# Performance work log

Measured on AMD Instinct MI355X. Metric: run time of the kernel, lower is better.

The kernel has to match this reference:

```python
import jax, jax.numpy as jnp
import numpy as np

NG, NT, E = 2500, 20000, 640000
SRC_DIM, DST_DIM, HID, OUT, NCLS = 128, 500, 128, 128, 16


def setup_inputs() -> dict:
    key = jax.random.key(0)
    ks = jax.random.split(key, 11)
    d = {
        "gene_feats": jax.random.normal(ks[0], (NG, SRC_DIM), jnp.float32),
        "train_feats": jax.random.normal(ks[1], (NT, DST_DIM), jnp.float32),
        "edge_src": jax.random.randint(ks[2], (E,), 0, NG),
        "edge_dst": jax.random.randint(ks[3], (E,), 0, NT),
        # conv1: SAGEConv((src_dim, dst_dim) -> hidden)
        "W1_neigh": jax.random.normal(ks[4], (SRC_DIM, HID), jnp.float32) / np.sqrt(SRC_DIM),
        "W1_self": jax.random.normal(ks[5], (DST_DIM, HID), jnp.float32) / np.sqrt(DST_DIM),
        "b1": jnp.zeros((HID,), jnp.float32),
        # conv2: SAGEConv(hidden -> out); src input is the raw gene features
        "W2_neigh": jax.random.normal(ks[6], (HID, OUT), jnp.float32) / np.sqrt(HID),
        "W2_self": jax.random.normal(ks[7], (HID, OUT), jnp.float32) / np.sqrt(HID),
        "b2": jnp.zeros((OUT,), jnp.float32),
        # classifier MLP
        "Wc1": jax.random.normal(ks[8], (OUT, OUT), jnp.float32) / np.sqrt(OUT),
        "bc1": jnp.zeros((OUT,), jnp.float32),
        "Wc2": jax.random.normal(ks[9], (OUT, NCLS), jnp.float32) / np.sqrt(OUT),
        "bc2": jnp.zeros((NCLS,), jnp.float32),
    }
    return d


def _segment_mean(msgs, dst, num_segments):
    # mean over in-edges; isolated dst nodes get 0 (DGL convention)
    sums = jax.ops.segment_sum(msgs, dst, num_segments=num_segments)
    cnt = jax.ops.segment_sum(jnp.ones((msgs.shape[0],), msgs.dtype), dst,
                              num_segments=num_segments)
    return sums / jnp.maximum(cnt, 1.0)[:, None]


def reference(gene_feats, train_feats, edge_src, edge_dst,
              W1_neigh, W1_self, b1, W2_neigh, W2_self, b2,
              Wc1, bc1, Wc2, bc2):
    # mean-aggregate gene (src) features onto train (dst) nodes
    agg = _segment_mean(gene_feats[edge_src], edge_dst, NT)  # [NT, SRC_DIM]
    # conv1: fc_self(h_dst) + fc_neigh(mean_neigh) + bias, then ReLU
    h1 = jax.nn.relu(train_feats @ W1_self + agg @ W1_neigh + b1)  # [NT, HID]
    # conv2 reuses raw gene features as src -> same mean aggregation
    h2 = jax.nn.relu(h1 @ W2_self + agg @ W2_neigh + b2)  # [NT, OUT]
    # classifier: Linear -> ReLU -> Linear
    return jax.nn.relu(h2 @ Wc1 + bc1) @ Wc2 + bc2  # [NT, NCLS]
```

## Files before the change

### kernel.cpp

```cpp
#include <hip/hip_runtime.h>


#define NG 2500
#define NT 20000
#define NE 640000
#define NCLS 16
#define CAP 96

typedef unsigned short u16;
typedef unsigned int u32;

typedef float f32x4 __attribute__((ext_vector_type(4)));
typedef __bf16 bf16x8 __attribute__((ext_vector_type(8)));

__device__ __forceinline__ float b2f(u16 u) { return __uint_as_float(((u32)u) << 16); }
__device__ __forceinline__ float blo(u32 p) { return __uint_as_float(p << 16); }
__device__ __forceinline__ float bhi(u32 p) { return __uint_as_float(p & 0xffff0000u); }
__device__ __forceinline__ u16 f2b(float f) {
    u32 u = __float_as_uint(f);
    return (u16)((u + 0x7fffu + ((u >> 16) & 1u)) >> 16);
}

#define B1N 81920
#define B2N 32768
#define B3N 16384
#define B4N 2048
#define NEB 625
#define GNB 625
#define PKB 520

__global__ __launch_bounds__(256) void k_prep(
    const int* __restrict__ esrc, const int* __restrict__ edst,
    int* __restrict__ cnt, u16* __restrict__ csr,
    const float* __restrict__ gene, u32* __restrict__ GH32,
    const float* __restrict__ W1n, const float* __restrict__ W1s,
    const float* __restrict__ W2n, const float* __restrict__ W2s,
    const float* __restrict__ Wc1, const float* __restrict__ Wc2,
    u16* __restrict__ B1h, u16* __restrict__ B1l,
    u16* __restrict__ B2h, u16* __restrict__ B2l,
    u16* __restrict__ B3h, u16* __restrict__ B3l,
    u16* __restrict__ B4h, u16* __restrict__ B4l) {
    int blk = blockIdx.x, t = threadIdx.x;
    if (blk < NEB) {
        int e0 = (blk * 256 + t) * 4;
        const int4 s4 = *(const int4*)(esrc + e0);
        const int4 d4 = *(const int4*)(edst + e0);
        int ss[4] = {s4.x, s4.y, s4.z, s4.w};
        int dd[4] = {d4.x, d4.y, d4.z, d4.w};
#pragma unroll
        for (int i = 0; i < 4; ++i) {
            unsigned d = (unsigned)dd[i];
            if (d < NT) {
                int slot = atomicAdd(&cnt[d], 1);
                if (slot < CAP) csr[(size_t)d * CAP + slot] = (u16)ss[i];
            }
        }
        return;
    }
    if (blk < NEB + GNB) {
        int idx = (blk - NEB) * 256 + t;
        float2 v = ((const float2*)gene)[idx];
        GH32[idx] = (u32)f2b(v.x) | ((u32)f2b(v.y) << 16);
        return;
    }
    int idx = (blk - NEB - GNB) * 256 + t;
    float v = 0.f;
    u16 *ph = 0, *pl = 0;
    int off = 0;
    if (idx < B1N) {
        int j = idx & 7, l = (idx >> 3) & 63, rest = idx >> 9;
        int g = rest & 7, kk = rest >> 3;
        int k = kk * 32 + ((l >> 4) << 3) + j, n = (g << 4) + (l & 15);
        if (k < 500) v = W1s[k * 128 + n];
        else if (k >= 512) v = W1n[(k - 512) * 128 + n];
        ph = B1h; pl = B1l; off = idx;
    } else if (idx < B1N + B2N) {
        int e = idx - B1N;
        int j = e & 7, l = (e >> 3) & 63, rest = e >> 9;
        int g = rest & 7, kk = rest >> 3;
        int k = kk * 32 + ((l >> 4) << 3) + j, n = (g << 4) + (l & 15);
        v = (k < 128) ? W2s[k * 128 + n] : W2n[(k - 128) * 128 + n];
        ph = B2h; pl = B2l; off = e;
    } else if (idx < B1N + B2N + B3N) {
        int e = idx - (B1N + B2N);
        int j = e & 7, l = (e >> 3) & 63, rest = e >> 9;
        int g = rest & 7, kk = rest >> 3;
        int k = kk * 32 + ((l >> 4) << 3) + j, n = (g << 4) + (l & 15);
        v = Wc1[k * 128 + n];
        ph = B3h; pl = B3l; off = e;
    } else if (idx < B1N + B2N + B3N + B4N) {
        int e = idx - (B1N + B2N + B3N);
        int j = e & 7, l = (e >> 3) & 63, kk = e >> 9;
        int k = kk * 32 + ((l >> 4) << 3) + j, n = l & 15;
        v = Wc2[k * 16 + n];
        ph = B4h; pl = B4l; off = e;
    }
    if (ph) {
        u16 hi = f2b(v);
        u16 lo = f2b(v - b2f(hi));
        ph[off] = hi;
        pl[off] = lo;
    }
}

__global__ __launch_bounds__(512) void k_mega(
    const int* __restrict__ cnt, const u16* __restrict__ csr,
    const u16* __restrict__ GH, const float* __restrict__ train,
    const u16* __restrict__ B1h, const u16* __restrict__ B1l,
    const u16* __restrict__ B2h, const u16* __restrict__ B2l,
    const u16* __restrict__ B3h, const u16* __restrict__ B3l,
    const u16* __restrict__ B4h, const u16* __restrict__ B4l,
    const float* __restrict__ b1, const float* __restrict__ b2,
    const float* __restrict__ bc1, const float* __restrict__ bc2,
    float* __restrict__ out) {
    __shared__ __align__(16) u16 SMEM[26112];
    u16* SAGh = SMEM;
    u16* SAGl = SMEM + 4352;
    u16* S1h = SMEM + 8704;
    u16* S1l = SMEM + 13056;
    u16* S2h = SMEM + 17408;
    u16* S2l = SMEM + 21760;
    u16* TS = SMEM + 8704;

    int t = threadIdx.x;
    int row0 = blockIdx.x * 32;

    float4 st[8];
    {
        const float4* tb = (const float4*)(train + (size_t)row0 * 500);
#pragma unroll
        for (int i = 0; i < 7; ++i) st[i] = tb[t + i * 512];
        if (t < 416) st[7] = tb[t + 3584];
    }

    {
        int r = t >> 4, cg = t & 15;
        int d = row0 + r;
        int ctrue = cnt[d];
        int c = ctrue > CAP ? CAP : ctrue;
        const u16* crow = csr + (size_t)d * CAP;
        float a[8];
#pragma unroll
        for (int p = 0; p < 8; ++p) a[p] = 0.f;
        int j = 0;
        for (; j + 1 < c; j += 2) {
            int s0 = crow[j], s1 = crow[j + 1];
            uint4 p0 = *(const uint4*)(GH + (size_t)s0 * 128 + cg * 8);
            uint4 p1 = *(const uint4*)(GH + (size_t)s1 * 128 + cg * 8);
            a[0] += blo(p0.x); a[1] += bhi(p0.x);
            a[2] += blo(p0.y); a[3] += bhi(p0.y);
            a[4] += blo(p0.z); a[5] += bhi(p0.z);
            a[6] += blo(p0.w); a[7] += bhi(p0.w);
            a[0] += blo(p1.x); a[1] += bhi(p1.x);
            a[2] += blo(p1.y); a[3] += bhi(p1.y);
            a[4] += blo(p1.z); a[5] += bhi(p1.z);
            a[6] += blo(p1.w); a[7] += bhi(p1.w);
        }
        if (j < c) {
            int s = crow[j];
            uint4 p0 = *(const uint4*)(GH + (size_t)s * 128 + cg * 8);
            a[0] += blo(p0.x); a[1] += bhi(p0.x);
            a[2] += blo(p0.y); a[3] += bhi(p0.y);
            a[4] += blo(p0.z); a[5] += bhi(p0.z);
            a[6] += blo(p0.w); a[7] += bhi(p0.w);
        }
        float inv = (ctrue > 0) ? 1.f / (float)ctrue : 0.f;
        int base = (r * 136 + cg * 8) >> 1;
        u32* SH = (u32*)SAGh;
        u32* SL = (u32*)SAGl;
#pragma unroll
        for (int p = 0; p < 4; ++p) {
            float x = a[2 * p] * inv, y = a[2 * p + 1] * inv;
            u16 hx = f2b(x), hy = f2b(y);
            SH[base + p] = (u32)hx | ((u32)hy << 16);
            SL[base + p] = (u32)f2b(x - b2f(hx)) | ((u32)f2b(y - b2f(hy)) << 16);
        }
    }

    {
        u32* T32 = (u32*)TS;
#pragma unroll
        for (int i = 0; i < 8; ++i) {
            int idx = t + i * 512;
            if (i == 7 && t >= 416) break;
            int r = idx / 125, c4 = idx - r * 125;
            int base = r * 260 + c4 * 2;
            T32[base] = (u32)f2b(st[i].x) | ((u32)f2b(st[i].y) << 16);
            T32[base + 1] = (u32)f2b(st[i].z) | ((u32)f2b(st[i].w) << 16);
        }
        if (t < 192) {
            int r = t / 6, c = t - r * 6;
            T32[r * 260 + 250 + c] = 0;
        }
    }
    __syncthreads();

    int lane = t & 63, g = t >> 6;
    int m = lane & 15, q = lane >> 4, n16 = lane & 15;

    int hr0 = m * 136 + q * 8;
    int hr1 = (16 + m) * 136 + q * 8;
    int cr0 = q * 4, cr1 = 16 + q * 4;
    const f32x4 z4 = {0.f, 0.f, 0.f, 0.f};
    f32x4 acc0 = z4, acc1 = z4;

    const u16* tA0 = TS + m * 520 + q * 8;
    const u16* tA1 = TS + (16 + m) * 520 + q * 8;
#pragma unroll
    for (int kk = 0; kk < 16; ++kk) {
        bf16x8 a0 = *(const bf16x8*)(tA0 + kk * 32);
        bf16x8 a1 = *(const bf16x8*)(tA1 + kk * 32);
        size_t bo = ((size_t)(kk * 8 + g) * 64 + lane) * 8;
        bf16x8 bh = *(const bf16x8*)(B1h + bo);
        bf16x8 bl = *(const bf16x8*)(B1l + bo);
        acc0 = __builtin_amdgcn_mfma_f32_16x16x32_bf16(a0, bh, acc0, 0, 0, 0);
        acc0 = __builtin_amdgcn_mfma_f32_16x16x32_bf16(a0, bl, acc0, 0, 0, 0);
        acc1 = __builtin_amdgcn_mfma_f32_16x16x32_bf16(a1, bh, acc1, 0, 0, 0);
        acc1 = __builtin_amdgcn_mfma_f32_16x16x32_bf16(a1, bl, acc1, 0, 0, 0);
    }
#pragma unroll
    for (int kk = 16; kk < 20; ++kk) {
        int o = (kk - 16) * 32;
        bf16x8 ah0 = *(const bf16x8*)(SAGh + hr0 + o);
        bf16x8 al0 = *(const bf16x8*)(SAGl + hr0 + o);
        bf16x8 ah1 = *(const bf16x8*)(SAGh + hr1 + o);
        bf16x8 al1 = *(const bf16x8*)(SAGl + hr1 + o);
        size_t bo = ((size_t)(kk * 8 + g) * 64 + lane) * 8;
        bf16x8 bh = *(const bf16x8*)(B1h + bo);
        bf16x8 bl = *(const bf16x8*)(B1l + bo);
        acc0 = __builtin_amdgcn_mfma_f32_16x16x32_bf16(ah0, bh, acc0, 0, 0, 0);
        acc0 = __builtin_amdgcn_mfma_f32_16x16x32_bf16(ah0, bl, acc0, 0, 0, 0);
        acc0 = __builtin_amdgcn_mfma_f32_16x16x32_bf16(al0, bh, acc0, 0, 0, 0);
        acc1 = __builtin_amdgcn_mfma_f32_16x16x32_bf16(ah1, bh, acc1, 0, 0, 0);
        acc1 = __builtin_amdgcn_mfma_f32_16x16x32_bf16(ah1, bl, acc1, 0, 0, 0);
        acc1 = __builtin_amdgcn_mfma_f32_16x16x32_bf16(al1, bh, acc1, 0, 0, 0);
    }
    __syncthreads();
    {
        int n = g * 16 + n16;
        float bias = b1[n];
#pragma unroll
        for (int rg = 0; rg < 4; ++rg) {
            float v0 = acc0[rg] + bias; v0 = v0 > 0.f ? v0 : 0.f;
            float v1 = acc1[rg] + bias; v1 = v1 > 0.f ? v1 : 0.f;
            u16 h0 = f2b(v0), h1v = f2b(v1);
            S1h[(cr0 + rg) * 136 + n] = h0; S1l[(cr0 + rg) * 136 + n] = f2b(v0 - b2f(h0));
            S1h[(cr1 + rg) * 136 + n] = h1v; S1l[(cr1 + rg) * 136 + n] = f2b(v1 - b2f(h1v));
        }
    }
    __syncthreads();

    acc0 = z4; acc1 = z4;
#pragma unroll
    for (int kk = 0; kk < 8; ++kk) {
        const u16* Ph = (kk < 4) ? S1h : SAGh;
        const u16* Pl = (kk < 4) ? S1l : SAGl;
        int o = (kk & 3) * 32;
        bf16x8 ah0 = *(const bf16x8*)(Ph + hr0 + o);
        bf16x8 al0 = *(const bf16x8*)(Pl + hr0 + o);
        bf16x8 ah1 = *(const bf16x8*)(Ph + hr1 + o);
        bf16x8 al1 = *(const bf16x8*)(Pl + hr1 + o);
        size_t bo = ((size_t)(kk * 8 + g) * 64 + lane) * 8;
        bf16x8 bh = *(const bf16x8*)(B2h + bo);
        bf16x8 bl = *(const bf16x8*)(B2l + bo);
        acc0 = __builtin_amdgcn_mfma_f32_16x16x32_bf16(ah0, bh, acc0, 0, 0, 0);
        acc0 = __builtin_amdgcn_mfma_f32_16x16x32_bf16(ah0, bl, acc0, 0, 0, 0);
        acc0 = __builtin_amdgcn_mfma_f32_16x16x32_bf16(al0, bh, acc0, 0, 0, 0);
        acc1 = __builtin_amdgcn_mfma_f32_16x16x32_bf16(ah1, bh, acc1, 0, 0, 0);
        acc1 = __builtin_amdgcn_mfma_f32_16x16x32_bf16(ah1, bl, acc1, 0, 0, 0);
        acc1 = __builtin_amdgcn_mfma_f32_16x16x32_bf16(al1, bh, acc1, 0, 0, 0);
    }
    {
        int n = g * 16 + n16;
        float bias = b2[n];
#pragma unroll
        for (int rg = 0; rg < 4; ++rg) {
            float v0 = acc0[rg] + bias; v0 = v0 > 0.f ? v0 : 0.f;
            float v1 = acc1[rg] + bias; v1 = v1 > 0.f ? v1 : 0.f;
            u16 h0 = f2b(v0), h1v = f2b(v1);
            S2h[(cr0 + rg) * 136 + n] = h0; S2l[(cr0 + rg) * 136 + n] = f2b(v0 - b2f(h0));
            S2h[(cr1 + rg) * 136 + n] = h1v; S2l[(cr1 + rg) * 136 + n] = f2b(v1 - b2f(h1v));
        }
    }
    __syncthreads();

    acc0 = z4; acc1 = z4;
#pragma unroll
    for (int kk = 0; kk < 4; ++kk) {
        int o = kk * 32;
        bf16x8 ah0 = *(const bf16x8*)(S2h + hr0 + o);
        bf16x8 al0 = *(const bf16x8*)(S2l + hr0 + o);
        bf16x8 ah1 = *(const bf16x8*)(S2h + hr1 + o);
        bf16x8 al1 = *(const bf16x8*)(S2l + hr1 + o);
        size_t bo = ((size_t)(kk * 8 + g) * 64 + lane) * 8;
        bf16x8 bh = *(const bf16x8*)(B3h + bo);
        bf16x8 bl = *(const bf16x8*)(B3l + bo);
        acc0 = __builtin_amdgcn_mfma_f32_16x16x32_bf16(ah0, bh, acc0, 0, 0, 0);
        acc0 = __builtin_amdgcn_mfma_f32_16x16x32_bf16(ah0, bl, acc0, 0, 0, 0);
        acc0 = __builtin_amdgcn_mfma_f32_16x16x32_bf16(al0, bh, acc0, 0, 0, 0);
        acc1 = __builtin_amdgcn_mfma_f32_16x16x32_bf16(ah1, bh, acc1, 0, 0, 0);
        acc1 = __builtin_amdgcn_mfma_f32_16x16x32_bf16(ah1, bl, acc1, 0, 0, 0);
        acc1 = __builtin_amdgcn_mfma_f32_16x16x32_bf16(al1, bh, acc1, 0, 0, 0);
    }
    {
        int n = g * 16 + n16;
        float bias = bc1[n];
#pragma unroll
        for (int rg = 0; rg < 4; ++rg) {
            float v0 = acc0[rg] + bias; v0 = v0 > 0.f ? v0 : 0.f;
            float v1 = acc1[rg] + bias; v1 = v1 > 0.f ? v1 : 0.f;
            u16 h0 = f2b(v0), h1v = f2b(v1);
            S1h[(cr0 + rg) * 136 + n] = h0; S1l[(cr0 + rg) * 136 + n] = f2b(v0 - b2f(h0));
            S1h[(cr1 + rg) * 136 + n] = h1v; S1l[(cr1 + rg) * 136 + n] = f2b(v1 - b2f(h1v));
        }
    }
    __syncthreads();

    if (g < 2) {
        int hr = (g == 0) ? hr0 : hr1;
        int cr = (g == 0) ? cr0 : cr1;
        f32x4 a4 = z4;
#pragma unroll
        for (int kk = 0; kk < 4; ++kk) {
            bf16x8 ah = *(const bf16x8*)(S1h + hr + kk * 32);
            bf16x8 al = *(const bf16x8*)(S1l + hr + kk * 32);
            size_t bo = ((size_t)kk * 64 + lane) * 8;
            bf16x8 bh = *(const bf16x8*)(B4h + bo);
            bf16x8 bl = *(const bf16x8*)(B4l + bo);
            a4 = __builtin_amdgcn_mfma_f32_16x16x32_bf16(ah, bh, a4, 0, 0, 0);
            a4 = __builtin_amdgcn_mfma_f32_16x16x32_bf16(ah, bl, a4, 0, 0, 0);
            a4 = __builtin_amdgcn_mfma_f32_16x16x32_bf16(al, bh, a4, 0, 0, 0);
        }
        float bias = bc2[n16];
#pragma unroll
        for (int rg = 0; rg < 4; ++rg)
            out[(size_t)(row0 + cr + rg) * NCLS + n16] = a4[rg] + bias;
    }
}

extern "C" void kernel_launch(void* const* d_in, const int* in_sizes, int n_in,
                              void* d_out, int out_size, void* d_ws, size_t ws_size,
                              hipStream_t stream) {
    const float* gene = (const float*)d_in[0];
    const float* train = (const float*)d_in[1];
    const int* esrc = (const int*)d_in[2];
    const int* edst = (const int*)d_in[3];

    char* ws = (char*)d_ws;
    int* cnt = (int*)(ws + 0);
    u16* csr = (u16*)(ws + 80000);
    u16* GH = (u16*)(ws + 3920000);
    u16* B1h = (u16*)(ws + 4560000);
    u16* B1l = (u16*)(ws + 4723840);
    u16* B2h = (u16*)(ws + 4887680);
    u16* B2l = (u16*)(ws + 4953216);
    u16* B3h = (u16*)(ws + 5018752);
    u16* B3l = (u16*)(ws + 5051520);
    u16* B4h = (u16*)(ws + 5084288);
    u16* B4l = (u16*)(ws + 5088384);

    hipMemsetAsync(cnt, 0, NT * sizeof(int), stream);
    k_prep<<<NEB + GNB + PKB, 256, 0, stream>>>(
        esrc, edst, cnt, csr, gene, (u32*)GH,
        (const float*)d_in[4], (const float*)d_in[5], (const float*)d_in[7],
        (const float*)d_in[8], (const float*)d_in[10], (const float*)d_in[12],
        B1h, B1l, B2h, B2l, B3h, B3l, B4h, B4l);
    k_mega<<<NT / 32, 512, 0, stream>>>(
        cnt, csr, GH, train, B1h, B1l, B2h, B2l, B3h, B3l, B4h, B4l,
        (const float*)d_in[6], (const float*)d_in[9], (const float*)d_in[11],
        (const float*)d_in[13], (float*)d_out);
}
```

Before: 167.6 us.

## Halve rows per block in fused GNN kernel and batch eight edges per thread

The fused kernel now processes 16 destination rows per 512-thread block instead of 32. That halves shared memory and register use and doubles the grid to 1250 blocks for better occupancy and load balance. The trade-off is that each block reloads the full weight tiles for half as many rows, which doubles weight traffic per row, and each MFMA stage now has a single accumulator chain. Separately, the edge-bucketing phase handles eight edges per thread with fewer blocks.

```diff
diff --git a/kernel.cpp b/kernel.cpp
--- a/kernel.cpp
+++ b/kernel.cpp
@@ -25,7 +25,7 @@
 #define B2N 32768
 #define B3N 16384
 #define B4N 2048
-#define NEB 625
+#define NEB 313
 #define GNB 625
 #define PKB 520
 
@@ -42,17 +42,21 @@
     u16* __restrict__ B4h, u16* __restrict__ B4l) {
     int blk = blockIdx.x, t = threadIdx.x;
     if (blk < NEB) {
-        int e0 = (blk * 256 + t) * 4;
-        const int4 s4 = *(const int4*)(esrc + e0);
-        const int4 d4 = *(const int4*)(edst + e0);
-        int ss[4] = {s4.x, s4.y, s4.z, s4.w};
-        int dd[4] = {d4.x, d4.y, d4.z, d4.w};
-#pragma unroll
-        for (int i = 0; i < 4; ++i) {
-            unsigned d = (unsigned)dd[i];
-            if (d < NT) {
-                int slot = atomicAdd(&cnt[d], 1);
-                if (slot < CAP) csr[(size_t)d * CAP + slot] = (u16)ss[i];
+        int e0 = (blk * 256 + t) * 8;
+        if (e0 < NE) {
+            int4 sA = *(const int4*)(esrc + e0);
+            int4 sB = *(const int4*)(esrc + e0 + 4);
+            int4 dA = *(const int4*)(edst + e0);
+            int4 dB = *(const int4*)(edst + e0 + 4);
+            int ss[8] = {sA.x, sA.y, sA.z, sA.w, sB.x, sB.y, sB.z, sB.w};
+            int dd[8] = {dA.x, dA.y, dA.z, dA.w, dB.x, dB.y, dB.z, dB.w};
+#pragma unroll
+            for (int i = 0; i < 8; ++i) {
+                unsigned d = (unsigned)dd[i];
+                if (d < NT) {
+                    int slot = atomicAdd(&cnt[d], 1);
+                    if (slot < CAP) csr[(size_t)d * CAP + slot] = (u16)ss[i];
+                }
             }
         }
         return;
@@ -113,82 +117,96 @@
     const float* __restrict__ b1, const float* __restrict__ b2,
     const float* __restrict__ bc1, const float* __restrict__ bc2,
     float* __restrict__ out) {
-    __shared__ __align__(16) u16 SMEM[26112];
+    __shared__ __align__(16) u16 SMEM[13056];
     u16* SAGh = SMEM;
-    u16* SAGl = SMEM + 4352;
-    u16* S1h = SMEM + 8704;
-    u16* S1l = SMEM + 13056;
-    u16* S2h = SMEM + 17408;
-    u16* S2l = SMEM + 21760;
-    u16* TS = SMEM + 8704;
+    u16* SAGl = SMEM + 2176;
+    u16* S1h = SMEM + 4352;
+    u16* S1l = SMEM + 6528;
+    u16* S2h = SMEM + 8704;
+    u16* S2l = SMEM + 10880;
+    u16* TS = SMEM + 4352;
 
     int t = threadIdx.x;
-    int row0 = blockIdx.x * 32;
-
-    float4 st[8];
+    int row0 = blockIdx.x * 16;
+
+    float4 st0, st1, st2, st3;
     {
         const float4* tb = (const float4*)(train + (size_t)row0 * 500);
-#pragma unroll
-        for (int i = 0; i < 7; ++i) st[i] = tb[t + i * 512];
-        if (t < 416) st[7] = tb[t + 3584];
-    }
-
-    {
-        int r = t >> 4, cg = t & 15;
+        st0 = tb[t];
+        st1 = tb[t + 512];
+        st2 = tb[t + 1024];
+        int i3 = (t < 464) ? (t + 1536) : 0;
+        st3 = tb[i3];
+    }
+
+    {
+        int r = t >> 5, cg = t & 31;
         int d = row0 + r;
         int ctrue = cnt[d];
         int c = ctrue > CAP ? CAP : ctrue;
         const u16* crow = csr + (size_t)d * CAP;
-        float a[8];
-#pragma unroll
-        for (int p = 0; p < 8; ++p) a[p] = 0.f;
+        float a0 = 0.f, a1 = 0.f, a2 = 0.f, a3 = 0.f;
         int j = 0;
         for (; j + 1 < c; j += 2) {
             int s0 = crow[j], s1 = crow[j + 1];
-            uint4 p0 = *(const uint4*)(GH + (size_t)s0 * 128 + cg * 8);
-            uint4 p1 = *(const uint4*)(GH + (size_t)s1 * 128 + cg * 8);
-            a[0] += blo(p0.x); a[1] += bhi(p0.x);
-            a[2] += blo(p0.y); a[3] += bhi(p0.y);
-            a[4] += blo(p0.z); a[5] += bhi(p0.z);
-            a[6] += blo(p0.w); a[7] += bhi(p0.w);
-            a[0] += blo(p1.x); a[1] += bhi(p1.x);
-            a[2] += blo(p1.y); a[3] += bhi(p1.y);
-            a[4] += blo(p1.z); a[5] += bhi(p1.z);
-            a[6] += blo(p1.w); a[7] += bhi(p1.w);
+            uint2 p0 = *(const uint2*)(GH + (size_t)s0 * 128 + cg * 4);
+            uint2 p1 = *(const uint2*)(GH + (size_t)s1 * 128 + cg * 4);
+            a0 += blo(p0.x); a1 += bhi(p0.x);
+            a2 += blo(p0.y); a3 += bhi(p0.y);
+            a0 += blo(p1.x); a1 += bhi(p1.x);
+            a2 += blo(p1.y); a3 += bhi(p1.y);
         }
         if (j < c) {
             int s = crow[j];
-            uint4 p0 = *(const uint4*)(GH + (size_t)s * 128 + cg * 8);
-            a[0] += blo(p0.x); a[1] += bhi(p0.x);
-            a[2] += blo(p0.y); a[3] += bhi(p0.y);
-            a[4] += blo(p0.z); a[5] += bhi(p0.z);
-            a[6] += blo(p0.w); a[7] += bhi(p0.w);
+            uint2 p0 = *(const uint2*)(GH + (size_t)s * 128 + cg * 4);
+            a0 += blo(p0.x); a1 += bhi(p0.x);
+            a2 += blo(p0.y); a3 += bhi(p0.y);
         }
         float inv = (ctrue > 0) ? 1.f / (float)ctrue : 0.f;
-        int base = (r * 136 + cg * 8) >> 1;
+        int base = r * 68 + cg * 2;
         u32* SH = (u32*)SAGh;
         u32* SL = (u32*)SAGl;
-#pragma unroll
-        for (int p = 0; p < 4; ++p) {
-            float x = a[2 * p] * inv, y = a[2 * p + 1] * inv;
-            u16 hx = f2b(x), hy = f2b(y);
-            SH[base + p] = (u32)hx | ((u32)hy << 16);
-            SL[base + p] = (u32)f2b(x - b2f(hx)) | ((u32)f2b(y - b2f(hy)) << 16);
-        }
+        float x = a0 * inv, y = a1 * inv;
+        u16 hx = f2b(x), hy = f2b(y);
+        SH[base] = (u32)hx | ((u32)hy << 16);
+        SL[base] = (u32)f2b(x - b2f(hx)) | ((u32)f2b(y - b2f(hy)) << 16);
+        x = a2 * inv; y = a3 * inv;
+        hx = f2b(x); hy = f2b(y);
+        SH[base + 1] = (u32)hx | ((u32)hy << 16);
+        SL[base + 1] = (u32)f2b(x - b2f(hx)) | ((u32)f2b(y - b2f(hy)) << 16);
     }
 
     {
         u32* T32 = (u32*)TS;
-#pragma unroll
-        for (int i = 0; i < 8; ++i) {
-            int idx = t + i * 512;
-            if (i == 7 && t >= 416) break;
+        int idx = t;
+        {
             int r = idx / 125, c4 = idx - r * 125;
             int base = r * 260 + c4 * 2;
-            T32[base] = (u32)f2b(st[i].x) | ((u32)f2b(st[i].y) << 16);
-            T32[base + 1] = (u32)f2b(st[i].z) | ((u32)f2b(st[i].w) << 16);
-        }
-        if (t < 192) {
+            T32[base] = (u32)f2b(st0.x) | ((u32)f2b(st0.y) << 16);
+            T32[base + 1] = (u32)f2b(st0.z) | ((u32)f2b(st0.w) << 16);
+        }
+        idx = t + 512;
+        {
+            int r = idx / 125, c4 = idx - r * 125;
+            int base = r * 260 + c4 * 2;
+            T32[base] = (u32)f2b(st1.x) | ((u32)f2b(st1.y) << 16);
+            T32[base + 1] = (u32)f2b(st1.z) | ((u32)f2b(st1.w) << 16);
+        }
+        idx = t + 1024;
+        {
+            int r = idx / 125, c4 = idx - r * 125;
+            int base = r * 260 + c4 * 2;
+            T32[base] = (u32)f2b(st2.x) | ((u32)f2b(st2.y) << 16);
+            T32[base + 1] = (u32)f2b(st2.z) | ((u32)f2b(st2.w) << 16);
+        }
+        if (t < 464) {
+            idx = t + 1536;
+            int r = idx / 125, c4 = idx - r * 125;
+            int base = r * 260 + c4 * 2;
+            T32[base] = (u32)f2b(st3.x) | ((u32)f2b(st3.y) << 16);
+            T32[base + 1] = (u32)f2b(st3.z) | ((u32)f2b(st3.w) << 16);
+        }
+        if (t < 96) {
             int r = t / 6, c = t - r * 6;
             T32[r * 260 + 250 + c] = 0;
         }
@@ -199,41 +217,31 @@
     int m = lane & 15, q = lane >> 4, n16 = lane & 15;
 
     int hr0 = m * 136 + q * 8;
-    int hr1 = (16 + m) * 136 + q * 8;
-    int cr0 = q * 4, cr1 = 16 + q * 4;
+    int cr0 = q * 4;
     const f32x4 z4 = {0.f, 0.f, 0.f, 0.f};
-    f32x4 acc0 = z4, acc1 = z4;
+    f32x4 acc0 = z4;
 
     const u16* tA0 = TS + m * 520 + q * 8;
-    const u16* tA1 = TS + (16 + m) * 520 + q * 8;
 #pragma unroll
     for (int kk = 0; kk < 16; ++kk) {
         bf16x8 a0 = *(const bf16x8*)(tA0 + kk * 32);
-        bf16x8 a1 = *(const bf16x8*)(tA1 + kk * 32);
         size_t bo = ((size_t)(kk * 8 + g) * 64 + lane) * 8;
         bf16x8 bh = *(const bf16x8*)(B1h + bo);
         bf16x8 bl = *(const bf16x8*)(B1l + bo);
         acc0 = __builtin_amdgcn_mfma_f32_16x16x32_bf16(a0, bh, acc0, 0, 0, 0);
         acc0 = __builtin_amdgcn_mfma_f32_16x16x32_bf16(a0, bl, acc0, 0, 0, 0);
-        acc1 = __builtin_amdgcn_mfma_f32_16x16x32_bf16(a1, bh, acc1, 0, 0, 0);
-        acc1 = __builtin_amdgcn_mfma_f32_16x16x32_bf16(a1, bl, acc1, 0, 0, 0);
     }
 #pragma unroll
     for (int kk = 16; kk < 20; ++kk) {
         int o = (kk - 16) * 32;
         bf16x8 ah0 = *(const bf16x8*)(SAGh + hr0 + o);
         bf16x8 al0 = *(const bf16x8*)(SAGl + hr0 + o);
-        bf16x8 ah1 = *(const bf16x8*)(SAGh + hr1 + o);
-        bf16x8 al1 = *(const bf16x8*)(SAGl + hr1 + o);
         size_t bo = ((size_t)(kk * 8 + g) * 64 + lane) * 8;
         bf16x8 bh = *(const bf16x8*)(B1h + bo);
         bf16x8 bl = *(const bf16x8*)(B1l + bo);
         acc0 = __builtin_amdgcn_mfma_f32_16x16x32_bf16(ah0, bh, acc0, 0, 0, 0);
         acc0 = __builtin_amdgcn_mfma_f32_16x16x32_bf16(ah0, bl, acc0, 0, 0, 0);
         acc0 = __builtin_amdgcn_mfma_f32_16x16x32_bf16(al0, bh, acc0, 0, 0, 0);
-        acc1 = __builtin_amdgcn_mfma_f32_16x16x32_bf16(ah1, bh, acc1, 0, 0, 0);
-        acc1 = __builtin_amdgcn_mfma_f32_16x16x32_bf16(ah1, bl, acc1, 0, 0, 0);
-        acc1 = __builtin_amdgcn_mfma_f32_16x16x32_bf16(al1, bh, acc1, 0, 0, 0);
     }
     __syncthreads();
     {
@@ -242,15 +250,14 @@
 #pragma unroll
         for (int rg = 0; rg < 4; ++rg) {
             float v0 = acc0[rg] + bias; v0 = v0 > 0.f ? v0 : 0.f;
-            float v1 = acc1[rg] + bias; v1 = v1 > 0.f ? v1 : 0.f;
-            u16 h0 = f2b(v0), h1v = f2b(v1);
-            S1h[(cr0 + rg) * 136 + n] = h0; S1l[(cr0 + rg) * 136 + n] = f2b(v0 - b2f(h0));
-            S1h[(cr1 + rg) * 136 + n] = h1v; S1l[(cr1 + rg) * 136 + n] = f2b(v1 - b2f(h1v));
-        }
-    }
-    __syncthreads();
-
-    acc0 = z4; acc1 = z4;
+            u16 h0 = f2b(v0);
+            S1h[(cr0 + rg) * 136 + n] = h0;
+            S1l[(cr0 + rg) * 136 + n] = f2b(v0 - b2f(h0));
+        }
+    }
+    __syncthreads();
+
+    acc0 = z4;
 #pragma unroll
     for (int kk = 0; kk < 8; ++kk) {
         const u16* Ph = (kk < 4) ? S1h : SAGh;
@@ -258,17 +265,12 @@
         int o = (kk & 3) * 32;
         bf16x8 ah0 = *(const bf16x8*)(Ph + hr0 + o);
         bf16x8 al0 = *(const bf16x8*)(Pl + hr0 + o);
-        bf16x8 ah1 = *(const bf16x8*)(Ph + hr1 + o);
-        bf16x8 al1 = *(const bf16x8*)(Pl + hr1 + o);
         size_t bo = ((size_t)(kk * 8 + g) * 64 + lane) * 8;
         bf16x8 bh = *(const bf16x8*)(B2h + bo);
         bf16x8 bl = *(const bf16x8*)(B2l + bo);
         acc0 = __builtin_amdgcn_mfma_f32_16x16x32_bf16(ah0, bh, acc0, 0, 0, 0);
         acc0 = __builtin_amdgcn_mfma_f32_16x16x32_bf16(ah0, bl, acc0, 0, 0, 0);
         acc0 = __builtin_amdgcn_mfma_f32_16x16x32_bf16(al0, bh, acc0, 0, 0, 0);
-        acc1 = __builtin_amdgcn_mfma_f32_16x16x32_bf16(ah1, bh, acc1, 0, 0, 0);
-        acc1 = __builtin_amdgcn_mfma_f32_16x16x32_bf16(ah1, bl, acc1, 0, 0, 0);
-        acc1 = __builtin_amdgcn_mfma_f32_16x16x32_bf16(al1, bh, acc1, 0, 0, 0);
     }
     {
         int n = g * 16 + n16;
@@ -276,31 +278,25 @@
 #pragma unroll
         for (int rg = 0; rg < 4; ++rg) {
             float v0 = acc0[rg] + bias; v0 = v0 > 0.f ? v0 : 0.f;
-            float v1 = acc1[rg] + bias; v1 = v1 > 0.f ? v1 : 0.f;
-            u16 h0 = f2b(v0), h1v = f2b(v1);
-            S2h[(cr0 + rg) * 136 + n] = h0; S2l[(cr0 + rg) * 136 + n] = f2b(v0 - b2f(h0));
-            S2h[(cr1 + rg) * 136 + n] = h1v; S2l[(cr1 + rg) * 136 + n] = f2b(v1 - b2f(h1v));
-        }
-    }
-    __syncthreads();
-
-    acc0 = z4; acc1 = z4;
+            u16 h0 = f2b(v0);
+            S2h[(cr0 + rg) * 136 + n] = h0;
+            S2l[(cr0 + rg) * 136 + n] = f2b(v0 - b2f(h0));
+        }
+    }
+    __syncthreads();
+
+    acc0 = z4;
 #pragma unroll
     for (int kk = 0; kk < 4; ++kk) {
         int o = kk * 32;
         bf16x8 ah0 = *(const bf16x8*)(S2h + hr0 + o);
         bf16x8 al0 = *(const bf16x8*)(S2l + hr0 + o);
-        bf16x8 ah1 = *(const bf16x8*)(S2h + hr1 + o);
-        bf16x8 al1 = *(const bf16x8*)(S2l + hr1 + o);
         size_t bo = ((size_t)(kk * 8 + g) * 64 + lane) * 8;
         bf16x8 bh = *(const bf16x8*)(B3h + bo);
         bf16x8 bl = *(const bf16x8*)(B3l + bo);
         acc0 = __builtin_amdgcn_mfma_f32_16x16x32_bf16(ah0, bh, acc0, 0, 0, 0);
         acc0 = __builtin_amdgcn_mfma_f32_16x16x32_bf16(ah0, bl, acc0, 0, 0, 0);
         acc0 = __builtin_amdgcn_mfma_f32_16x16x32_bf16(al0, bh, acc0, 0, 0, 0);
-        acc1 = __builtin_amdgcn_mfma_f32_16x16x32_bf16(ah1, bh, acc1, 0, 0, 0);
-        acc1 = __builtin_amdgcn_mfma_f32_16x16x32_bf16(ah1, bl, acc1, 0, 0, 0);
-        acc1 = __builtin_amdgcn_mfma_f32_16x16x32_bf16(al1, bh, acc1, 0, 0, 0);
     }
     {
         int n = g * 16 + n16;
@@ -308,22 +304,19 @@
 #pragma unroll
         for (int rg = 0; rg < 4; ++rg) {
             float v0 = acc0[rg] + bias; v0 = v0 > 0.f ? v0 : 0.f;
-            float v1 = acc1[rg] + bias; v1 = v1 > 0.f ? v1 : 0.f;
-            u16 h0 = f2b(v0), h1v = f2b(v1);
-            S1h[(cr0 + rg) * 136 + n] = h0; S1l[(cr0 + rg) * 136 + n] = f2b(v0 - b2f(h0));
-            S1h[(cr1 + rg) * 136 + n] = h1v; S1l[(cr1 + rg) * 136 + n] = f2b(v1 - b2f(h1v));
-        }
-    }
-    __syncthreads();
-
-    if (g < 2) {
-        int hr = (g == 0) ? hr0 : hr1;
-        int cr = (g == 0) ? cr0 : cr1;
+            u16 h0 = f2b(v0);
+            S1h[(cr0 + rg) * 136 + n] = h0;
+            S1l[(cr0 + rg) * 136 + n] = f2b(v0 - b2f(h0));
+        }
+    }
+    __syncthreads();
+
+    if (g == 0) {
         f32x4 a4 = z4;
 #pragma unroll
         for (int kk = 0; kk < 4; ++kk) {
-            bf16x8 ah = *(const bf16x8*)(S1h + hr + kk * 32);
-            bf16x8 al = *(const bf16x8*)(S1l + hr + kk * 32);
+            bf16x8 ah = *(const bf16x8*)(S1h + hr0 + kk * 32);
+            bf16x8 al = *(const bf16x8*)(S1l + hr0 + kk * 32);
             size_t bo = ((size_t)kk * 64 + lane) * 8;
             bf16x8 bh = *(const bf16x8*)(B4h + bo);
             bf16x8 bl = *(const bf16x8*)(B4l + bo);
@@ -334,7 +327,7 @@
         float bias = bc2[n16];
 #pragma unroll
         for (int rg = 0; rg < 4; ++rg)
-            out[(size_t)(row0 + cr + rg) * NCLS + n16] = a4[rg] + bias;
+            out[(size_t)(row0 + cr0 + rg) * NCLS + n16] = a4[rg] + bias;
     }
 }
 
@@ -365,7 +358,7 @@
         (const float*)d_in[4], (const float*)d_in[5], (const float*)d_in[7],
         (const float*)d_in[8], (const float*)d_in[10], (const float*)d_in[12],
         B1h, B1l, B2h, B2l, B3h, B3l, B4h, B4l);
-    k_mega<<<NT / 32, 512, 0, stream>>>(
+    k_mega<<<NT / 16, 512, 0, stream>>>(
         cnt, csr, GH, train, B1h, B1l, B2h, B2l, B3h, B3l, B4h, B4l,
         (const float*)d_in[6], (const float*)d_in[9], (const float*)d_in[11],
         (const float*)d_in[13], (float*)d_out);
```

Result: slower. 180.4 us (+7.6%).

## Interleave neighbor gather with train-feature MFMA and batch index loads

Applied to the files above, without the earlier changes.

The mean-aggregation gather no longer runs as its own phase before the GEMM. Its loads are now issued in batches of eight rows, with the indices read as uint4 vectors, and these batches are interleaved with the first sixteen K-steps of the train-feature MFMA loop. The goal is to hide gather memory latency behind matrix work and keep more loads in flight per thread. The synchronisation is moved so the aggregation results are published only before the aggregated-feature K-steps. The kernel also requests three blocks per CU via launch bounds, which tightens the register budget and could cause spills given the eight live uint4 buffers.

```diff
diff --git a/kernel.cpp b/kernel.cpp
--- a/kernel.cpp
+++ b/kernel.cpp
@@ -103,7 +103,7 @@
     }
 }
 
-__global__ __launch_bounds__(512) void k_mega(
+__global__ __launch_bounds__(512, 3) void k_mega(
     const int* __restrict__ cnt, const u16* __restrict__ csr,
     const u16* __restrict__ GH, const float* __restrict__ train,
     const u16* __restrict__ B1h, const u16* __restrict__ B1l,
@@ -133,49 +133,19 @@
         if (t < 416) st[7] = tb[t + 3584];
     }
 
-    {
-        int r = t >> 4, cg = t & 15;
-        int d = row0 + r;
-        int ctrue = cnt[d];
-        int c = ctrue > CAP ? CAP : ctrue;
-        const u16* crow = csr + (size_t)d * CAP;
-        float a[8];
-#pragma unroll
-        for (int p = 0; p < 8; ++p) a[p] = 0.f;
-        int j = 0;
-        for (; j + 1 < c; j += 2) {
-            int s0 = crow[j], s1 = crow[j + 1];
-            uint4 p0 = *(const uint4*)(GH + (size_t)s0 * 128 + cg * 8);
-            uint4 p1 = *(const uint4*)(GH + (size_t)s1 * 128 + cg * 8);
-            a[0] += blo(p0.x); a[1] += bhi(p0.x);
-            a[2] += blo(p0.y); a[3] += bhi(p0.y);
-            a[4] += blo(p0.z); a[5] += bhi(p0.z);
-            a[6] += blo(p0.w); a[7] += bhi(p0.w);
-            a[0] += blo(p1.x); a[1] += bhi(p1.x);
-            a[2] += blo(p1.y); a[3] += bhi(p1.y);
-            a[4] += blo(p1.z); a[5] += bhi(p1.z);
-            a[6] += blo(p1.w); a[7] += bhi(p1.w);
-        }
-        if (j < c) {
-            int s = crow[j];
-            uint4 p0 = *(const uint4*)(GH + (size_t)s * 128 + cg * 8);
-            a[0] += blo(p0.x); a[1] += bhi(p0.x);
-            a[2] += blo(p0.y); a[3] += bhi(p0.y);
-            a[4] += blo(p0.z); a[5] += bhi(p0.z);
-            a[6] += blo(p0.w); a[7] += bhi(p0.w);
-        }
-        float inv = (ctrue > 0) ? 1.f / (float)ctrue : 0.f;
-        int base = (r * 136 + cg * 8) >> 1;
-        u32* SH = (u32*)SAGh;
-        u32* SL = (u32*)SAGl;
-#pragma unroll
-        for (int p = 0; p < 4; ++p) {
-            float x = a[2 * p] * inv, y = a[2 * p + 1] * inv;
-            u16 hx = f2b(x), hy = f2b(y);
-            SH[base + p] = (u32)hx | ((u32)hy << 16);
-            SL[base + p] = (u32)f2b(x - b2f(hx)) | ((u32)f2b(y - b2f(hy)) << 16);
-        }
-    }
+    int gr = t >> 4, cg = t & 15;
+    int d = row0 + gr;
+    int ctrue = cnt[d];
+    int c = ctrue > CAP ? CAP : ctrue;
+    const u16* crow = csr + (size_t)d * CAP;
+    int nfull = c >> 3;
+    uint4 i40 = *(const uint4*)(crow);
+    uint4 i41 = *(const uint4*)(crow + 8);
+    uint4 i42 = *(const uint4*)(crow + 16);
+    uint4 i43 = *(const uint4*)(crow + 24);
+    float a[8];
+#pragma unroll
+    for (int p = 0; p < 8; ++p) a[p] = 0.f;
 
     {
         u32* T32 = (u32*)TS;
@@ -189,8 +159,8 @@
             T32[base + 1] = (u32)f2b(st[i].z) | ((u32)f2b(st[i].w) << 16);
         }
         if (t < 192) {
-            int r = t / 6, c = t - r * 6;
-            T32[r * 260 + 250 + c] = 0;
+            int r = t / 6, c4 = t - r * 6;
+            T32[r * 260 + 250 + c4] = 0;
         }
     }
     __syncthreads();
@@ -203,21 +173,95 @@
     int cr0 = q * 4, cr1 = 16 + q * 4;
     const f32x4 z4 = {0.f, 0.f, 0.f, 0.f};
     f32x4 acc0 = z4, acc1 = z4;
-
     const u16* tA0 = TS + m * 520 + q * 8;
     const u16* tA1 = TS + (16 + m) * 520 + q * 8;
-#pragma unroll
-    for (int kk = 0; kk < 16; ++kk) {
-        bf16x8 a0 = *(const bf16x8*)(tA0 + kk * 32);
-        bf16x8 a1 = *(const bf16x8*)(tA1 + kk * 32);
-        size_t bo = ((size_t)(kk * 8 + g) * 64 + lane) * 8;
-        bf16x8 bh = *(const bf16x8*)(B1h + bo);
-        bf16x8 bl = *(const bf16x8*)(B1l + bo);
-        acc0 = __builtin_amdgcn_mfma_f32_16x16x32_bf16(a0, bh, acc0, 0, 0, 0);
-        acc0 = __builtin_amdgcn_mfma_f32_16x16x32_bf16(a0, bl, acc0, 0, 0, 0);
-        acc1 = __builtin_amdgcn_mfma_f32_16x16x32_bf16(a1, bh, acc1, 0, 0, 0);
-        acc1 = __builtin_amdgcn_mfma_f32_16x16x32_bf16(a1, bl, acc1, 0, 0, 0);
-    }
+
+#define ACC(p)                                      \
+    do {                                            \
+        a[0] += blo((p).x); a[1] += bhi((p).x);     \
+        a[2] += blo((p).y); a[3] += bhi((p).y);     \
+        a[4] += blo((p).z); a[5] += bhi((p).z);     \
+        a[6] += blo((p).w); a[7] += bhi((p).w);     \
+    } while (0)
+
+    auto GHLoad = [&](int s) -> uint4 {
+        return *(const uint4*)(GH + (size_t)s * 128 + cg * 8);
+    };
+    uint4 P0, P1, P2, P3, P4, P5, P6, P7;
+    auto issue8 = [&](uint4 iq) {
+        P0 = GHLoad((int)(iq.x & 0xffffu)); P1 = GHLoad((int)(iq.x >> 16));
+        P2 = GHLoad((int)(iq.y & 0xffffu)); P3 = GHLoad((int)(iq.y >> 16));
+        P4 = GHLoad((int)(iq.z & 0xffffu)); P5 = GHLoad((int)(iq.z >> 16));
+        P6 = GHLoad((int)(iq.w & 0xffffu)); P7 = GHLoad((int)(iq.w >> 16));
+    };
+    auto acc8 = [&]() {
+        ACC(P0); ACC(P1); ACC(P2); ACC(P3);
+        ACC(P4); ACC(P5); ACC(P6); ACC(P7);
+    };
+    auto kk4 = [&](int base) {
+#pragma unroll
+        for (int kk = base; kk < base + 4; ++kk) {
+            bf16x8 a0 = *(const bf16x8*)(tA0 + kk * 32);
+            bf16x8 a1 = *(const bf16x8*)(tA1 + kk * 32);
+            size_t bo = ((size_t)(kk * 8 + g) * 64 + lane) * 8;
+            bf16x8 bh = *(const bf16x8*)(B1h + bo);
+            bf16x8 bl = *(const bf16x8*)(B1l + bo);
+            acc0 = __builtin_amdgcn_mfma_f32_16x16x32_bf16(a0, bh, acc0, 0, 0, 0);
+            acc0 = __builtin_amdgcn_mfma_f32_16x16x32_bf16(a0, bl, acc0, 0, 0, 0);
+            acc1 = __builtin_amdgcn_mfma_f32_16x16x32_bf16(a1, bh, acc1, 0, 0, 0);
+            acc1 = __builtin_amdgcn_mfma_f32_16x16x32_bf16(a1, bl, acc1, 0, 0, 0);
+        }
+    };
+
+    if (nfull > 0) issue8(i40);
+    kk4(0);
+    if (nfull > 0) acc8();
+    if (nfull > 1) issue8(i41);
+    kk4(4);
+    if (nfull > 1) acc8();
+    if (nfull > 2) issue8(i42);
+    kk4(8);
+    if (nfull > 2) acc8();
+    if (nfull > 3) issue8(i43);
+    kk4(12);
+    if (nfull > 3) acc8();
+    for (int b = 4; b < nfull; ++b) {
+        uint4 i4 = *(const uint4*)(crow + b * 8);
+        issue8(i4);
+        acc8();
+    }
+    {
+        int j = nfull * 8;
+        if (j < c) {
+            uint4 i4 = *(const uint4*)(crow + j);
+            u32 w[4] = {i4.x, i4.y, i4.z, i4.w};
+#pragma unroll
+            for (int k = 0; k < 8; ++k) {
+                int s = (int)((w[k >> 1] >> ((k & 1) * 16)) & 0xffffu);
+                bool live = (j + k) < c;
+                s = live ? s : 0;
+                uint4 p = GHLoad(s);
+                if (live) ACC(p);
+            }
+        }
+    }
+#undef ACC
+
+    {
+        float inv = (ctrue > 0) ? 1.f / (float)ctrue : 0.f;
+        int base = (gr * 136 + cg * 8) >> 1;
+        u32* SH = (u32*)SAGh;
+        u32* SL = (u32*)SAGl;
+#pragma unroll
+        for (int p = 0; p < 4; ++p) {
+            float x = a[2 * p] * inv, y = a[2 * p + 1] * inv;
+            u16 hx = f2b(x), hy = f2b(y);
+            SH[base + p] = (u32)hx | ((u32)hy << 16);
+            SL[base + p] = (u32)f2b(x - b2f(hx)) | ((u32)f2b(y - b2f(hy)) << 16);
+        }
+    }
+    __syncthreads();
+
 #pragma unroll
     for (int kk = 16; kk < 20; ++kk) {
         int o = (kk - 16) * 32;
@@ -235,7 +279,6 @@
         acc1 = __builtin_amdgcn_mfma_f32_16x16x32_bf16(ah1, bl, acc1, 0, 0, 0);
         acc1 = __builtin_amdgcn_mfma_f32_16x16x32_bf16(al1, bh, acc1, 0, 0, 0);
     }
-    __syncthreads();
     {
         int n = g * 16 + n16;
         float bias = b1[n];
```

Result: slower. 172.5 us (+2.9%).
